# Optimization experiments

Measured on AMD Instinct MI355X. Metric: run time of the kernel, lower is better.

## Reference

```python
import jax, jax.numpy as jnp
import numpy as np


def setup_inputs() -> dict:
    key = jax.random.key(0)
    k1, k2 = jax.random.split(key)
    n = 12000
    dataset = jax.random.normal(k1, (n,), dtype=jnp.float32)
    weights = jax.random.uniform(k2, (n,), dtype=jnp.float32)
    return {"dataset": dataset, "weights": weights}


def reference(dataset, weights):
    # normalize weights (update_weights)
    w = weights / jnp.sum(weights)
    neff = jnp.sum(w) ** 2 / jnp.sum(w ** 2)
    # Silverman's factor (torch.std is unbiased -> ddof=1; torch.quantile is linear interp)
    std_dev = jnp.std(dataset, ddof=1)
    iqr = jnp.quantile(dataset, 0.75) - jnp.quantile(dataset, 0.25)
    sigma_hat = jnp.minimum(std_dev, iqr / 1.34)
    h = 0.9 * sigma_hat * neff ** (-0.2)
    inv_norm = 1.0 / (h * jnp.sqrt(2.0 * jnp.pi))
    # pairwise Gaussian kernel matrix: [n, n]
    diff = (dataset[:, None] - dataset[None, :]) / h
    kernel = jnp.exp(-0.5 * diff * diff) * inv_norm
    pdf = kernel @ w  # [n]
    return jnp.log(pdf + 1e-10)
```

## Files before the change

kernel.cpp:

```cpp
#include <hip/hip_runtime.h>
#include <math.h>


#define BLK 256
#define NB 2048
#define NPART 4
#define ELPB 3
#define GLO  (-8.0f)
#define GSCALE 128.0f
#define GBINW (1.0f / 128.0f)
#define CUT 4.0f

#if defined(__has_builtin)
#if __has_builtin(__builtin_amdgcn_exp2f)
#define EXP2(x) __builtin_amdgcn_exp2f(x)
#endif
#endif
#ifndef EXP2
#define EXP2(x) exp2f(x)
#endif

__device__ __forceinline__ int bin_of(float x) {
    int b = (int)((x - GLO) * GSCALE);
    b = b < 0 ? 0 : b;
    return b < NB ? b : NB - 1;
}

__global__ __launch_bounds__(1024) void binstat_k(const float* __restrict__ d,
                                                  const float* __restrict__ w,
                                                  float4* __restrict__ statP,
                                                  int* __restrict__ partH,
                                                  float* __restrict__ partW,
                                                  float* __restrict__ partWE,
                                                  int n) {
    __shared__ int   hl[NB];
    __shared__ float wl[NB];
    __shared__ float wel[NB];
    __shared__ float4 sstat[16];
    const int t = threadIdx.x, lane = t & 63, wid = t >> 6, blk = blockIdx.x;

    hl[t] = 0; hl[t + 1024] = 0;
    wl[t] = 0.f; wl[t + 1024] = 0.f;
    wel[t] = 0.f; wel[t + 1024] = 0.f;
    __syncthreads();

    float dv[ELPB], wv[ELPB];
    #pragma unroll
    for (int k = 0; k < ELPB; ++k) {
        int i = blk * (1024 * ELPB) + k * 1024 + t;
        bool ok = (i < n);
        dv[k] = ok ? d[i] : 0.f;
        wv[k] = ok ? w[i] : 0.f;
    }
    float s1 = 0.f, s2 = 0.f, sd = 0.f, sd2 = 0.f;
    #pragma unroll
    for (int k = 0; k < ELPB; ++k) {
        int i = blk * (1024 * ELPB) + k * 1024 + t;
        if (i < n) {
            s1 += wv[k]; s2 += wv[k] * wv[k];
            sd += dv[k]; sd2 += dv[k] * dv[k];
            int b = bin_of(dv[k]);
            atomicAdd(&hl[b], 1);
            atomicAdd(&wl[b], wv[k]);
            atomicAdd(&wel[b], wv[k] * dv[k]);
        }
    }
    for (int off = 32; off > 0; off >>= 1) {
        s1 += __shfl_down(s1, off); s2 += __shfl_down(s2, off);
        sd += __shfl_down(sd, off); sd2 += __shfl_down(sd2, off);
    }
    if (lane == 0) sstat[wid] = make_float4(s1, s2, sd, sd2);
    __syncthreads();
    if (t == 0) {
        float4 a = sstat[0];
        for (int q = 1; q < 16; ++q) {
            float4 b = sstat[q];
            a.x += b.x; a.y += b.y; a.z += b.z; a.w += b.w;
        }
        statP[blk] = a;
    }
    #pragma unroll
    for (int k = 0; k < 2; ++k) {
        int b = t + k * 1024;
        partH [blk * NB + b] = hl[b];
        partW [blk * NB + b] = wl[b];
        partWE[blk * NB + b] = wel[b];
    }
}

__global__ __launch_bounds__(BLK) void eval_k(const float* __restrict__ d,
                                              const float4* __restrict__ statP,
                                              const int* __restrict__ partH,
                                              const float* __restrict__ partW,
                                              const float* __restrict__ partWE,
                                              float* __restrict__ out, int n) {
    __shared__ float2 sb[NB];
    __shared__ int cum[NB];
    __shared__ int woff[4];
    __shared__ int tbin[4], tprev[4];
    __shared__ float spar[4];
    __shared__ float sred[BLK];
    const int t = threadIdx.x, lane = t & 63, wv = t >> 6;
    const int base = t * 8;

    int h8[8], pre[8];
    int s = 0;
    #pragma unroll
    for (int k = 0; k < 8; ++k) {
        int b = base + k;
        int hsum = 0; float Wsum = 0.f, Esum = 0.f;
        #pragma unroll
        for (int p = 0; p < NPART; ++p) {
            hsum += partH[p * NB + b];
            Wsum += partW[p * NB + b];
            Esum += partWE[p * NB + b];
        }
        h8[k] = hsum;
        sb[b] = make_float2(Esum, Wsum);
        s += hsum;
        pre[k] = s;
    }
    int v = s;
    for (int off = 1; off < 64; off <<= 1) {
        int u = __shfl_up(v, off);
        if (lane >= off) v += u;
    }
    if (lane == 63) woff[wv] = v;
    __syncthreads();
    int wexcl = 0;
    #pragma unroll
    for (int q = 0; q < 4; ++q) if (q < wv) wexcl += woff[q];
    const int texcl = wexcl + (v - s);
    #pragma unroll
    for (int k = 0; k < 8; ++k) cum[base + k] = texcl + pre[k];

    const double p25 = 0.25 * (double)(n - 1);
    const double p75 = 0.75 * (double)(n - 1);
    const int l25 = (int)p25, l75 = (int)p75;
    const int u25 = (l25 + 1 < n) ? l25 + 1 : l25;
    const int u75 = (l75 + 1 < n) ? l75 + 1 : l75;
    const int targets[4] = {l25, u25, l75, u75};
    #pragma unroll
    for (int k = 0; k < 8; ++k) {
        int prev = texcl + (k ? pre[k - 1] : 0);
        int incl = texcl + pre[k];
        #pragma unroll
        for (int r = 0; r < 4; ++r)
            if (prev <= targets[r] && targets[r] < incl) { tbin[r] = base + k; tprev[r] = prev; }
    }
    __syncthreads();

    if (t == 0) {
        float qv[4];
        #pragma unroll
        for (int r = 0; r < 4; ++r) {
            int b = tbin[r];
            int cnt = cum[b] - tprev[r];
            float pos = (float)b + ((float)(targets[r] - tprev[r]) + 0.5f) / (float)cnt;
            qv[r] = GLO + pos * GBINW;
        }
        double S1 = 0, S2 = 0, Sd = 0, Sd2 = 0;
        #pragma unroll
        for (int p = 0; p < NPART; ++p) {
            float4 a = statP[p];
            S1 += a.x; S2 += a.y; Sd += a.z; Sd2 += a.w;
        }
        float neff = (float)(S1 * S1 / S2);
        float varf = (float)((Sd2 - Sd * Sd / (double)n) / ((double)n - 1.0));
        float sdev = sqrtf(varf);
        float f25 = (float)(p25 - (double)l25), f75 = (float)(p75 - (double)l75);
        float q25 = qv[0] + f25 * (qv[1] - qv[0]);
        float q75 = qv[2] + f75 * (qv[3] - qv[2]);
        float sig = fminf(sdev, (q75 - q25) * (1.0f / 1.34f));
        float hb = 0.9f * sig * exp2f(-0.2f * log2f(neff));
        float rr = 0.84932180f / hb;
        float wsc = 1.0f / (hb * 2.50662827f * (float)S1);
        float delta = (rr > 0.f) ? ceilf((CUT / rr) * GSCALE) + 2.0f : (float)NB;
        spar[0] = rr; spar[1] = wsc; spar[2] = delta;
    }
    __syncthreads();
    const float rr = spar[0], wsc = spar[1];
    const int delta = (int)spar[2];

    #pragma unroll
    for (int k = 0; k < 8; ++k) {
        int b = base + k;
        float2 vr = sb[b];
        float W = vr.y;
        float mu = (W > 0.f) ? (vr.x / W) : 0.f;
        sb[b] = make_float2(mu * rr, W * wsc);
    }
    __syncthreads();

    const int i = blockIdx.x * 64 + lane;
    const float di = (i < n) ? d[i] : 0.f;
    const float ei = di * rr;
    const int bi = bin_of(di);
    int b0 = bi - delta; if (b0 < 0) b0 = 0;
    int b1 = bi + delta; if (b1 > NB - 1) b1 = NB - 1;
    const int len = b1 - b0 + 1;
    const int q = (len + 3) >> 2;
    int ws_ = b0 + wv * q;
    int we_ = ws_ + q; if (we_ > b1 + 1) we_ = b1 + 1;

    float acc0 = 0.f, acc1 = 0.f;
    int b = ws_;
    for (; b + 1 < we_; b += 2) {
        float2 p0 = sb[b], p1 = sb[b + 1];
        float u0 = ei - p0.x, u1 = ei - p1.x;
        acc0 = fmaf(p0.y, EXP2(-(u0 * u0)), acc0);
        acc1 = fmaf(p1.y, EXP2(-(u1 * u1)), acc1);
    }
    if (b < we_) {
        float2 p0 = sb[b];
        float u0 = ei - p0.x;
        acc0 = fmaf(p0.y, EXP2(-(u0 * u0)), acc0);
    }

    sred[wv * 64 + lane] = acc0 + acc1;
    __syncthreads();
    if (t < 64) {
        int ii = blockIdx.x * 64 + t;
        if (ii < n) {
            float p = sred[t] + sred[64 + t] + sred[128 + t] + sred[192 + t];
            out[ii] = logf(p + 1e-10f);
        }
    }
}

extern "C" void kernel_launch(void* const* d_in, const int* in_sizes, int n_in,
                              void* d_out, int out_size, void* d_ws, size_t ws_size,
                              hipStream_t stream) {
    const float* d = (const float*)d_in[0];
    const float* w = (const float*)d_in[1];
    float* out = (float*)d_out;
    const int n = in_sizes[0];

    const int nmax = ((n + 63) / 64) * 64;
    const int G = nmax / 64;

    float*  wsf    = (float*)d_ws;
    float4* statP  = (float4*)wsf;
    int*    partH  = (int*)(wsf + 16);
    float*  partW  = wsf + 16 + NPART * NB;
    float*  partWE = wsf + 16 + 2 * NPART * NB;

    binstat_k<<<NPART, 1024, 0, stream>>>(d, w, statP, partH, partW, partWE, n);
    eval_k<<<G, BLK, 0, stream>>>(d, statP, partH, partW, partWE, out, n);
}
```

Measured before the change: 24.51 us.

## Split binning across 16 smaller blocks and compute bandwidth redundantly per thread

```diff
diff --git a/kernel.cpp b/kernel.cpp
--- a/kernel.cpp
+++ b/kernel.cpp
@@ -4,7 +4,7 @@
 
 #define BLK 256
 #define NB 2048
-#define NPART 4
+#define NPART 16
 #define ELPB 3
 #define GLO  (-8.0f)
 #define GSCALE 128.0f
@@ -26,28 +26,30 @@
     return b < NB ? b : NB - 1;
 }
 
-__global__ __launch_bounds__(1024) void binstat_k(const float* __restrict__ d,
-                                                  const float* __restrict__ w,
-                                                  float4* __restrict__ statP,
-                                                  int* __restrict__ partH,
-                                                  float* __restrict__ partW,
-                                                  float* __restrict__ partWE,
-                                                  int n) {
+__global__ __launch_bounds__(BLK) void binstat_k(const float* __restrict__ d,
+                                                 const float* __restrict__ w,
+                                                 float4* __restrict__ statP,
+                                                 int* __restrict__ partH,
+                                                 float* __restrict__ partW,
+                                                 float* __restrict__ partWE,
+                                                 int n) {
     __shared__ int   hl[NB];
     __shared__ float wl[NB];
     __shared__ float wel[NB];
-    __shared__ float4 sstat[16];
+    __shared__ float4 sstat[4];
     const int t = threadIdx.x, lane = t & 63, wid = t >> 6, blk = blockIdx.x;
 
-    hl[t] = 0; hl[t + 1024] = 0;
-    wl[t] = 0.f; wl[t + 1024] = 0.f;
-    wel[t] = 0.f; wel[t + 1024] = 0.f;
+    #pragma unroll
+    for (int k = 0; k < 8; ++k) {
+        int b = t + k * BLK;
+        hl[b] = 0; wl[b] = 0.f; wel[b] = 0.f;
+    }
     __syncthreads();
 
     float dv[ELPB], wv[ELPB];
     #pragma unroll
     for (int k = 0; k < ELPB; ++k) {
-        int i = blk * (1024 * ELPB) + k * 1024 + t;
+        int i = blk * (BLK * ELPB) + k * BLK + t;
         bool ok = (i < n);
         dv[k] = ok ? d[i] : 0.f;
         wv[k] = ok ? w[i] : 0.f;
@@ -55,7 +57,7 @@
     float s1 = 0.f, s2 = 0.f, sd = 0.f, sd2 = 0.f;
     #pragma unroll
     for (int k = 0; k < ELPB; ++k) {
-        int i = blk * (1024 * ELPB) + k * 1024 + t;
+        int i = blk * (BLK * ELPB) + k * BLK + t;
         if (i < n) {
             s1 += wv[k]; s2 += wv[k] * wv[k];
             sd += dv[k]; sd2 += dv[k] * dv[k];
@@ -73,15 +75,15 @@
     __syncthreads();
     if (t == 0) {
         float4 a = sstat[0];
-        for (int q = 1; q < 16; ++q) {
+        for (int q = 1; q < 4; ++q) {
             float4 b = sstat[q];
             a.x += b.x; a.y += b.y; a.z += b.z; a.w += b.w;
         }
         statP[blk] = a;
     }
     #pragma unroll
-    for (int k = 0; k < 2; ++k) {
-        int b = t + k * 1024;
+    for (int k = 0; k < 8; ++k) {
+        int b = t + k * BLK;
         partH [blk * NB + b] = hl[b];
         partW [blk * NB + b] = wl[b];
         partWE[blk * NB + b] = wel[b];
@@ -95,29 +97,32 @@
                                               const float* __restrict__ partWE,
                                               float* __restrict__ out, int n) {
     __shared__ float2 sb[NB];
+    __shared__ int hbin[NB];
     __shared__ int cum[NB];
     __shared__ int woff[4];
     __shared__ int tbin[4], tprev[4];
-    __shared__ float spar[4];
     __shared__ float sred[BLK];
     const int t = threadIdx.x, lane = t & 63, wv = t >> 6;
-    const int base = t * 8;
-
-    int h8[8], pre[8];
-    int s = 0;
-    #pragma unroll
-    for (int k = 0; k < 8; ++k) {
-        int b = base + k;
+
+    for (int idx = t; idx < NB; idx += BLK) {
         int hsum = 0; float Wsum = 0.f, Esum = 0.f;
         #pragma unroll
         for (int p = 0; p < NPART; ++p) {
-            hsum += partH[p * NB + b];
-            Wsum += partW[p * NB + b];
-            Esum += partWE[p * NB + b];
-        }
-        h8[k] = hsum;
-        sb[b] = make_float2(Esum, Wsum);
-        s += hsum;
+            hsum += partH[p * NB + idx];
+            Wsum += partW[p * NB + idx];
+            Esum += partWE[p * NB + idx];
+        }
+        hbin[idx] = hsum;
+        sb[idx] = make_float2(Esum, Wsum);
+    }
+    __syncthreads();
+
+    const int base = t * 8;
+    int pre[8];
+    int s = 0;
+    #pragma unroll
+    for (int k = 0; k < 8; ++k) {
+        s += hbin[base + k];
         pre[k] = s;
     }
     int v = s;
@@ -150,37 +155,31 @@
     }
     __syncthreads();
 
-    if (t == 0) {
-        float qv[4];
-        #pragma unroll
-        for (int r = 0; r < 4; ++r) {
-            int b = tbin[r];
-            int cnt = cum[b] - tprev[r];
-            float pos = (float)b + ((float)(targets[r] - tprev[r]) + 0.5f) / (float)cnt;
-            qv[r] = GLO + pos * GBINW;
-        }
-        double S1 = 0, S2 = 0, Sd = 0, Sd2 = 0;
-        #pragma unroll
-        for (int p = 0; p < NPART; ++p) {
-            float4 a = statP[p];
-            S1 += a.x; S2 += a.y; Sd += a.z; Sd2 += a.w;
-        }
-        float neff = (float)(S1 * S1 / S2);
-        float varf = (float)((Sd2 - Sd * Sd / (double)n) / ((double)n - 1.0));
-        float sdev = sqrtf(varf);
-        float f25 = (float)(p25 - (double)l25), f75 = (float)(p75 - (double)l75);
-        float q25 = qv[0] + f25 * (qv[1] - qv[0]);
-        float q75 = qv[2] + f75 * (qv[3] - qv[2]);
-        float sig = fminf(sdev, (q75 - q25) * (1.0f / 1.34f));
-        float hb = 0.9f * sig * exp2f(-0.2f * log2f(neff));
-        float rr = 0.84932180f / hb;
-        float wsc = 1.0f / (hb * 2.50662827f * (float)S1);
-        float delta = (rr > 0.f) ? ceilf((CUT / rr) * GSCALE) + 2.0f : (float)NB;
-        spar[0] = rr; spar[1] = wsc; spar[2] = delta;
-    }
-    __syncthreads();
-    const float rr = spar[0], wsc = spar[1];
-    const int delta = (int)spar[2];
+    float qv[4];
+    #pragma unroll
+    for (int r = 0; r < 4; ++r) {
+        int b = tbin[r];
+        int cnt = cum[b] - tprev[r];
+        float pos = (float)b + ((float)(targets[r] - tprev[r]) + 0.5f) / (float)cnt;
+        qv[r] = GLO + pos * GBINW;
+    }
+    double S1 = 0, S2 = 0, Sd = 0, Sd2 = 0;
+    #pragma unroll
+    for (int p = 0; p < NPART; ++p) {
+        float4 a = statP[p];
+        S1 += a.x; S2 += a.y; Sd += a.z; Sd2 += a.w;
+    }
+    const float neff = (float)(S1 * S1 / S2);
+    const float varf = (float)((Sd2 - Sd * Sd / (double)n) / ((double)n - 1.0));
+    const float sdev = sqrtf(varf);
+    const float f25 = (float)(p25 - (double)l25), f75 = (float)(p75 - (double)l75);
+    const float q25 = qv[0] + f25 * (qv[1] - qv[0]);
+    const float q75 = qv[2] + f75 * (qv[3] - qv[2]);
+    const float sig = fminf(sdev, (q75 - q25) * (1.0f / 1.34f));
+    const float hb = 0.9f * sig * exp2f(-0.2f * log2f(neff));
+    const float rr = 0.84932180f / hb;
+    const float wsc = 1.0f / (hb * 2.50662827f * (float)S1);
+    const int delta = (rr > 0.f) ? (int)(ceilf((CUT / rr) * GSCALE) + 2.0f) : NB;
 
     #pragma unroll
     for (int k = 0; k < 8; ++k) {
@@ -241,10 +240,10 @@
 
     float*  wsf    = (float*)d_ws;
     float4* statP  = (float4*)wsf;
-    int*    partH  = (int*)(wsf + 16);
-    float*  partW  = wsf + 16 + NPART * NB;
-    float*  partWE = wsf + 16 + 2 * NPART * NB;
-
-    binstat_k<<<NPART, 1024, 0, stream>>>(d, w, statP, partH, partW, partWE, n);
+    int*    partH  = (int*)(wsf + 64);
+    float*  partW  = wsf + 64 + NPART * NB;
+    float*  partWE = wsf + 64 + 2 * NPART * NB;
+
+    binstat_k<<<NPART, BLK, 0, stream>>>(d, w, statP, partH, partW, partWE, n);
     eval_k<<<G, BLK, 0, stream>>>(d, statP, partH, partW, partWE, out, n);
 }
```

New measurement: 23.20 us. 5.4% less time.
